# Optimization experiments

Hardware: AMD Instinct MI355X
Metric: run time of the kernel (lower is better)

Reference implementation:

```python
import jax, jax.numpy as jnp
import numpy as np
import math

N, B, S = 2048, 4, 1024
SFZ, IFZ, H, A = 384, 256, 8, 64
LN_EPS = 1e-5


def setup_inputs() -> dict:
    key = jax.random.key(0)
    ks = jax.random.split(key, 12)
    x = jax.random.normal(ks[0], (N, IFZ), dtype=jnp.float32)
    emb = jax.random.normal(ks[1], (B, S, SFZ), dtype=jnp.float32)
    mask = jax.random.randint(ks[2], (B, S), 0, 2).astype(bool)
    batch = jnp.sort(jax.random.randint(ks[3], (N,), 0, B)).astype(jnp.int64)
    sc = 1.0 / math.sqrt(IFZ)
    scs = 1.0 / math.sqrt(SFZ)
    Wq = jax.random.normal(ks[4], (IFZ, H * A), dtype=jnp.float32) * sc
    Wk = jax.random.normal(ks[5], (SFZ, H * A), dtype=jnp.float32) * scs
    Wv = jax.random.normal(ks[6], (SFZ, H * A), dtype=jnp.float32) * scs
    Wg = jax.random.normal(ks[7], (IFZ, H * A), dtype=jnp.float32) * sc
    bg = jnp.zeros((H * A,), dtype=jnp.float32)
    Wback = jax.random.normal(ks[8], (H * A, IFZ), dtype=jnp.float32) / math.sqrt(H * A)
    bback = jnp.zeros((IFZ,), dtype=jnp.float32)
    gamma = jnp.ones((IFZ,), dtype=jnp.float32)
    beta = jnp.zeros((IFZ,), dtype=jnp.float32)
    return {"x": x, "packed_sequence_emb": emb, "packed_sequence_mask": mask,
            "batch": batch, "Wq": Wq, "Wk": Wk, "Wv": Wv, "Wg": Wg, "bg": bg,
            "Wback": Wback, "bback": bback, "gamma": gamma, "beta": beta}


def _masked_softmax(scores, mask):
    # scores: [N,S,H], mask: [N,S,1] bool; softmax over S with padded entries zeroed
    neg = jnp.finfo(scores.dtype).min
    s = jnp.where(mask, scores, neg)
    s = s - jnp.max(s, axis=1, keepdims=True)
    e = jnp.exp(s) * mask
    return e / (jnp.sum(e, axis=1, keepdims=True) + 1e-9)


def reference(x, packed_sequence_emb, packed_sequence_mask, batch,
              Wq, Wk, Wv, Wg, bg, Wback, bback, gamma, beta):
    scale = math.sqrt(A)
    q = (x @ Wq).reshape(N, H, A)                               # [N,H,A]
    k = (packed_sequence_emb @ Wk).reshape(B, S, H, A)          # [B,S,H,A]
    v = (packed_sequence_emb @ Wv).reshape(B, S, H, A)
    # scores per (node, candidate-batch), then gather node's own batch entry;
    # avoids materializing k[batch] of shape [N,S,H,A]
    scores_all = jnp.einsum('nha,bsha->nbsh', q, k) / scale     # [N,B,S,H]
    idx = batch[:, None, None, None].astype(jnp.int32)
    scores = jnp.take_along_axis(scores_all, idx, axis=1)[:, 0]  # [N,S,H]
    bmask = packed_sequence_mask[batch][..., None]               # [N,S,1]
    w = _masked_softmax(scores, bmask)                           # [N,S,H]
    feat_all = jnp.einsum('nsh,bsha->nbha', w, v)                # [N,B,H,A]
    feat = jnp.take_along_axis(feat_all, idx, axis=1)[:, 0]      # [N,H,A]
    gate = jax.nn.sigmoid(x @ Wg + bg).reshape(N, H, A)
    new = (gate * feat).reshape(N, H * A) @ Wback + bback        # [N,IFZ]
    y = math.sqrt(2.0) * x + new
    mu = jnp.mean(y, axis=-1, keepdims=True)
    var = jnp.mean((y - mu) ** 2, axis=-1, keepdims=True)
    out = (y - mu) * jax.lax.rsqrt(var + LN_EPS) * gamma + beta
    seq_aa_logits = jnp.sum(scores[..., :2], axis=-1)            # [N,S]
    return out, seq_aa_logits
```

## Files before the change

### kernel.cpp

```cpp
#include <hip/hip_runtime.h>
#include <hip/hip_bf16.h>

#define NND 2048
#define BBATCH 4
#define SS 1024
#define SFZ 384
#define IFZ 256
#define HH 8
#define AA 64
#define HA 512
#define NBX 48
#define NSPL 8

typedef __attribute__((ext_vector_type(8))) short bf16x8;
typedef __attribute__((ext_vector_type(4))) float f32x4;

__device__ __forceinline__ unsigned short f2bf(float f) {
    union { float f; unsigned u; } a; a.f = f;
    unsigned r = a.u + 0x7fffu + ((a.u >> 16) & 1u);
    return (unsigned short)(r >> 16);
}
__device__ __forceinline__ float bf2f(unsigned short u) {
    return __uint_as_float((unsigned)u << 16);
}

__device__ __forceinline__ bf16x8 cvt8(const float* __restrict__ p) {
    const float4 f0 = *(const float4*)p;
    const float4 f1 = *(const float4*)(p + 4);
    bf16x8 o;
    o[0] = (short)f2bf(f0.x); o[1] = (short)f2bf(f0.y);
    o[2] = (short)f2bf(f0.z); o[3] = (short)f2bf(f0.w);
    o[4] = (short)f2bf(f1.x); o[5] = (short)f2bf(f1.y);
    o[6] = (short)f2bf(f1.z); o[7] = (short)f2bf(f1.w);
    return o;
}

__device__ __forceinline__ void tile_transpose(
    const float* __restrict__ src, unsigned short* __restrict__ dst,
    int K, int N, int kt, int nt, int t)
{
    __shared__ unsigned short tile[64][65];
    const int k0 = kt * 64, n0 = nt * 64;
    const int tr = t >> 6, tc = t & 63;
    #pragma unroll
    for (int r = 0; r < 16; ++r)
        tile[tr + r*4][tc] = f2bf(src[(size_t)(k0 + tr + r*4) * N + n0 + tc]);
    __syncthreads();
    #pragma unroll
    for (int r = 0; r < 16; ++r)
        dst[(size_t)(n0 + tr + r*4) * K + k0 + tc] = tile[tc][tr + r*4];
}

__global__ __launch_bounds__(256) void prep_kernel(
    const float* __restrict__ Wk, const float* __restrict__ Wv,
    const float* __restrict__ Wq, const float* __restrict__ Wg,
    const float* __restrict__ Wback,
    const void* __restrict__ mask_raw, const void* __restrict__ batch_raw,
    unsigned short* __restrict__ WkT, unsigned short* __restrict__ WvT,
    unsigned short* __restrict__ WqT, unsigned short* __restrict__ WgT,
    unsigned short* __restrict__ WbackT,
    float* __restrict__ mask_f, int* __restrict__ seg)
{
    const int bx = blockIdx.x, t = threadIdx.x;
    if (bx < 48)  { tile_transpose(Wk, WkT, SFZ, HA, bx/8, bx%8, t); return; }
    if (bx < 96)  { const int i = bx-48;  tile_transpose(Wv, WvT, SFZ, HA, i/8, i%8, t); return; }
    if (bx < 128) { const int i = bx-96;  tile_transpose(Wq, WqT, IFZ, HA, i/8, i%8, t); return; }
    if (bx < 160) { const int i = bx-128; tile_transpose(Wg, WgT, IFZ, HA, i/8, i%8, t); return; }
    if (bx < 192) { const int i = bx-160; tile_transpose(Wback, WbackT, HA, IFZ, i/4, i%4, t); return; }
    __shared__ int fl[4];
    __shared__ int fb;
    __shared__ int cnt[4];
    if (t < 4) { fl[t] = 0; cnt[t] = 0; }
    if (t == 0) fb = 0;
    __syncthreads();
    const unsigned char*  mb = (const unsigned char*)mask_raw;
    const unsigned short* mh = (const unsigned short*)mask_raw;
    const unsigned int*   mw = (const unsigned int*)mask_raw;
    int f0 = 0, f1 = 0, f2 = 0, f3 = 0;
    for (int i = t; i < 2048; i += 256) {
        unsigned short h = mh[i];
        if (h == 0x3f80u) f0 = 1;
        if ((i & 1) == 0 && h != 0) f1 = 1;
    }
    for (int i = t; i < 4096; i += 256)
        if ((i & 3) != 0 && mb[i] != 0) f2 = 1;
    for (int i = t; i < 1024; i += 256)
        if ((i & 1) != 0 && mw[i] != 0) f3 = 1;
    const int* bw = (const int*)batch_raw;
    int f4 = 0;
    for (int i = t + 1; i < 2048; i += 256)
        if (bw[i] < bw[i-1]) f4 = 1;
    if (f0) atomicOr(&fl[0], 1);
    if (f1) atomicOr(&fl[1], 1);
    if (f2) atomicOr(&fl[2], 1);
    if (f3) atomicOr(&fl[3], 1);
    if (f4) atomicOr(&fb, 1);
    __syncthreads();
    int mode;
    if (fl[0])      mode = fl[1] ? 1 : 0;
    else if (fl[2]) mode = 2;
    else if (fl[3]) mode = 3;
    else            mode = 4;
    for (int s = t; s < BBATCH*SS; s += 256) {
        int m;
        switch (mode) {
            case 0:  m = (mw[s]   != 0); break;
            case 1:  m = (mh[s]   != 0); break;
            case 2:  m = (mb[s]   != 0); break;
            case 3:  m = (mw[s]   != 0); break;
            default: m = (mw[2*s] != 0); break;
        }
        mask_f[s] = m ? 1.0f : 0.0f;
    }
    const int b64 = fb;
    for (int i = t; i < NND; i += 256) {
        const int bv = (b64 ? bw[2*i] : bw[i]) & 3;
        atomicAdd(&cnt[bv], 1);
    }
    __syncthreads();
    if (t == 0) {
        int s = 0;
        for (int b = 0; b < 4; ++b) { seg[2*b] = s; s += cnt[b]; seg[2*b+1] = s; }
    }
}

__global__ __launch_bounds__(256) void proj_mfma(
    const float* __restrict__ emb, const float* __restrict__ x,
    const unsigned short* __restrict__ WkT, const unsigned short* __restrict__ WvT,
    const unsigned short* __restrict__ WqT, const unsigned short* __restrict__ WgT,
    const float* __restrict__ bg,
    unsigned short* __restrict__ k_blk, unsigned short* __restrict__ v_bf,
    unsigned short* __restrict__ q_bf, float* __restrict__ gate_ws)
{
    const int t = threadIdx.x, w = t >> 6, lane = t & 63;
    const int m16 = lane & 15, quad = lane >> 4;
    const int bx = blockIdx.x;
    if (bx < 512) {
        const int r0 = (bx >> 1) * 16;
        const int b = r0 >> 10, srow = r0 & (SS - 1);
        const float* ap = emb + (size_t)(r0 + m16) * SFZ + quad * 8;
        bf16x8 af[12];
        #pragma unroll
        for (int j = 0; j < 12; ++j) af[j] = cvt8(ap + j * 32);
        if ((bx & 1) == 0) {
            #pragma unroll
            for (int nt = 0; nt < 8; ++nt) {
                const int n0 = w * 128 + nt * 16;
                const unsigned short* bp = WkT + (size_t)(n0 + m16) * SFZ + quad * 8;
                f32x4 d = (f32x4){0.f, 0.f, 0.f, 0.f};
                #pragma unroll
                for (int j = 0; j < 12; ++j)
                    d = __builtin_amdgcn_mfma_f32_16x16x32_bf16(af[j], *(const bf16x8*)(bp + j * 32), d, 0, 0, 0);
                const int head = n0 >> 6, coff = (n0 & 63) + m16;
                unsigned short* kb = k_blk + (((size_t)(b * HH + head)) * SS) * 64 + coff;
                #pragma unroll
                for (int r = 0; r < 4; ++r)
                    kb[(size_t)(srow + quad * 4 + r) * 64] = f2bf(d[r]);
            }
        } else {
            #pragma unroll
            for (int nt = 0; nt < 8; ++nt) {
                const int n0 = w * 128 + nt * 16;
                const unsigned short* bp = WvT + (size_t)(n0 + m16) * SFZ + quad * 8;
                f32x4 d = (f32x4){0.f, 0.f, 0.f, 0.f};
                #pragma unroll
                for (int j = 0; j < 12; ++j)
                    d = __builtin_amdgcn_mfma_f32_16x16x32_bf16(af[j], *(const bf16x8*)(bp + j * 32), d, 0, 0, 0);
                #pragma unroll
                for (int r = 0; r < 4; ++r)
                    v_bf[(size_t)(r0 + quad * 4 + r) * HA + n0 + m16] = f2bf(d[r]);
            }
        }
    } else {
        const int i = bx - 512;
        const int r0 = (i >> 2) * 16;
        const int tensor = (i & 3) >> 1, half = i & 1;
        const unsigned short* Wt = tensor ? WgT : WqT;
        const float* ap = x + (size_t)(r0 + m16) * IFZ + quad * 8;
        bf16x8 af[8];
        #pragma unroll
        for (int j = 0; j < 8; ++j) af[j] = cvt8(ap + j * 32);
        #pragma unroll
        for (int nt = 0; nt < 4; ++nt) {
            const int n0 = half * 256 + w * 64 + nt * 16;
            const unsigned short* bp = Wt + (size_t)(n0 + m16) * IFZ + quad * 8;
            f32x4 d = (f32x4){0.f, 0.f, 0.f, 0.f};
            #pragma unroll
            for (int j = 0; j < 8; ++j)
                d = __builtin_amdgcn_mfma_f32_16x16x32_bf16(af[j], *(const bf16x8*)(bp + j * 32), d, 0, 0, 0);
            if (tensor == 0) {
                #pragma unroll
                for (int r = 0; r < 4; ++r)
                    q_bf[(size_t)(r0 + quad * 4 + r) * HA + n0 + m16] = f2bf(d[r]);
            } else {
                const float bgv = bg[n0 + m16];
                #pragma unroll
                for (int r = 0; r < 4; ++r)
                    gate_ws[(size_t)(r0 + quad * 4 + r) * HA + n0 + m16] =
                        1.f / (1.f + __expf(-(d[r] + bgv)));
            }
        }
    }
}

__global__ __launch_bounds__(256) void transpose_v(
    const unsigned short* __restrict__ v_bf, unsigned short* __restrict__ vT_bf)
{
    __shared__ unsigned short tile[64][65];
    const int t = threadIdx.x;
    const int s0 = blockIdx.x * 64, c0 = blockIdx.y * 64, b = blockIdx.z;
    const int tr = t >> 6, tc = t & 63;
    #pragma unroll
    for (int r = 0; r < 16; ++r)
        tile[tr + r*4][tc] = v_bf[(size_t)(b * SS + s0 + tr + r*4) * HA + c0 + tc];
    __syncthreads();
    #pragma unroll
    for (int r = 0; r < 16; ++r)
        vT_bf[((size_t)b * HA + c0 + tr + r*4) * SS + s0 + tc] = tile[tc][tr + r*4];
}

__global__ __launch_bounds__(256) void attn_kernel(
    const unsigned short* __restrict__ k_blk, const unsigned short* __restrict__ vT_bf,
    const unsigned short* __restrict__ q_bf, const float* __restrict__ mask_f,
    const int* __restrict__ seg, unsigned short* __restrict__ part_O,
    float2* __restrict__ part_ml, float* __restrict__ out_logits)
{
    __shared__ unsigned short P_lds[4][16][136];
    __shared__ float raw[2][16][132];
    const int bid = blockIdx.x;
    const int xcd = bid & 7;
    const int b   = xcd >> 1;
    const int idx = (bid >> 3) * 2 + (xcd & 1);
    const int z    = idx & 15;
    const int xblk = idx >> 4;
    const int hz    = z >> 3;
    const int split = z & 7;
    const int n0 = seg[2*b] + xblk * 16;
    const int nend = seg[2*b + 1];
    if (n0 >= nend) return;
    const int nvalid = min(16, nend - n0);

    const int t = threadIdx.x;
    const int w = t >> 6, lane = t & 63;
    const int m16 = lane & 15, quad = lane >> 4;
    const int h = hz * 4 + w;
    const int s0 = split * 128;

    int nq = n0 + m16; if (nq >= nend) nq = nend - 1;
    const unsigned short* qp = q_bf + (size_t)nq * HA + h * AA + quad * 8;
    const bf16x8 qa0 = *(const bf16x8*)qp;
    const bf16x8 qa1 = *(const bf16x8*)(qp + 32);

    const unsigned short* kb = k_blk + ((size_t)(b * HH + h)) * SS * 64;
    const unsigned short* vb = vT_bf + ((size_t)b * HA + h * AA) * SS;
    unsigned short (*Pw)[136] = P_lds[w];

    float msk[8];
    #pragma unroll
    for (int st = 0; st < 8; ++st)
        msk[st] = mask_f[b * SS + s0 + st * 16 + m16];

    f32x4 d[8];
    #pragma unroll
    for (int st = 0; st < 8; ++st) {
        const unsigned short* kp = kb + (size_t)(s0 + st * 16 + m16) * 64 + quad * 8;
        const bf16x8 b0 = *(const bf16x8*)kp;
        const bf16x8 b1 = *(const bf16x8*)(kp + 32);
        f32x4 acc = (f32x4){0.f, 0.f, 0.f, 0.f};
        acc = __builtin_amdgcn_mfma_f32_16x16x32_bf16(qa0, b0, acc, 0, 0, 0);
        acc = __builtin_amdgcn_mfma_f32_16x16x32_bf16(qa1, b1, acc, 0, 0, 0);
        #pragma unroll
        for (int r = 0; r < 4; ++r) acc[r] *= 0.125f;
        d[st] = acc;
    }
    if (hz == 0) {
        if (w < 2) {
            #pragma unroll
            for (int st = 0; st < 8; ++st)
                #pragma unroll
                for (int r = 0; r < 4; ++r)
                    raw[w][quad * 4 + r][st * 16 + m16] = d[st][r];
        }
        __syncthreads();
        for (int i = t; i < 16 * 128; i += 256) {
            const int node = i >> 7, sp = i & 127;
            if (node < nvalid)
                out_logits[(size_t)(n0 + node) * SS + s0 + sp] =
                    raw[0][node][sp] + raw[1][node][sp];
        }
    }
    float m_s[4], l_s[4];
    #pragma unroll
    for (int r = 0; r < 4; ++r) {
        float mx = -3.0e38f;
        #pragma unroll
        for (int st = 0; st < 8; ++st)
            mx = (msk[st] > 0.5f) ? fmaxf(mx, d[st][r]) : mx;
        mx = fmaxf(mx, __shfl_xor(mx, 1));
        mx = fmaxf(mx, __shfl_xor(mx, 2));
        mx = fmaxf(mx, __shfl_xor(mx, 4));
        mx = fmaxf(mx, __shfl_xor(mx, 8));
        m_s[r] = mx;
        float cs = 0.f;
        #pragma unroll
        for (int st = 0; st < 8; ++st) {
            const float e = (msk[st] > 0.5f) ? __expf(d[st][r] - mx) : 0.f;
            d[st][r] = e;
            cs += e;
        }
        cs += __shfl_xor(cs, 1);
        cs += __shfl_xor(cs, 2);
        cs += __shfl_xor(cs, 4);
        cs += __shfl_xor(cs, 8);
        l_s[r] = cs;
    }
    #pragma unroll
    for (int st = 0; st < 8; ++st)
        #pragma unroll
        for (int r = 0; r < 4; ++r)
            Pw[quad * 4 + r][st * 16 + m16] = f2bf(d[st][r]);
    f32x4 facc[4];
    #pragma unroll
    for (int a = 0; a < 4; ++a) facc[a] = (f32x4){0.f, 0.f, 0.f, 0.f};
    #pragma unroll
    for (int sub = 0; sub < 4; ++sub) {
        const bf16x8 pa = *(const bf16x8*)&Pw[m16][sub * 32 + quad * 8];
        const unsigned short* vp0 = vb + (size_t)m16 * SS + s0 + sub * 32 + quad * 8;
        #pragma unroll
        for (int a = 0; a < 4; ++a) {
            const bf16x8 vfr = *(const bf16x8*)(vp0 + (size_t)(a * 16) * SS);
            facc[a] = __builtin_amdgcn_mfma_f32_16x16x32_bf16(pa, vfr, facc[a], 0, 0, 0);
        }
    }
    unsigned short* po = part_O + (size_t)split * NND * HA;
    #pragma unroll
    for (int a = 0; a < 4; ++a)
        #pragma unroll
        for (int r = 0; r < 4; ++r) {
            const int row = quad * 4 + r;
            if (row < nvalid)
                po[(size_t)(n0 + row) * HA + h * AA + a * 16 + m16] = f2bf(facc[a][r]);
        }
    if (m16 == 0) {
        #pragma unroll
        for (int r = 0; r < 4; ++r) {
            const int row = quad * 4 + r;
            if (row < nvalid)
                part_ml[(size_t)split * NND * HH + (size_t)(n0 + row) * HH + h] =
                    make_float2(m_s[r], l_s[r]);
        }
    }
}

__global__ __launch_bounds__(256) void back_ln_fused(
    const unsigned short* __restrict__ part_O, const float2* __restrict__ part_ml,
    const float* __restrict__ gate_ws, const unsigned short* __restrict__ WbackT,
    const float* __restrict__ x, const float* __restrict__ bback,
    const float* __restrict__ gamma, const float* __restrict__ beta,
    float* __restrict__ out)
{
    __shared__ float coef[NSPL][8][8];
    __shared__ unsigned short gf_l[8][520];
    __shared__ float nl[8][260];
    const int t = threadIdx.x, w = t >> 6, lane = t & 63;
    const int m16 = lane & 15, quad = lane >> 4;
    const int r0 = blockIdx.x * 8;
    if (t < 64) {
        const int row = t >> 3, h = t & 7, n = r0 + row;
        float2 ml[NSPL];
        #pragma unroll
        for (int s = 0; s < NSPL; ++s)
            ml[s] = part_ml[(size_t)s * NND * HH + (size_t)n * HH + h];
        float M = -3.0e38f;
        #pragma unroll
        for (int s = 0; s < NSPL; ++s) M = fmaxf(M, ml[s].x);
        float L = 0.f;
        float e[NSPL];
        #pragma unroll
        for (int s = 0; s < NSPL; ++s) { e[s] = __expf(ml[s].x - M); L += ml[s].y * e[s]; }
        const float invL = 1.f / (L + 1e-9f);
        #pragma unroll
        for (int s = 0; s < NSPL; ++s) coef[s][row][h] = e[s] * invL;
    }
    __syncthreads();
    #pragma unroll
    for (int it = 0; it < 4; ++it) {
        const int i = (t + it * 256) * 4;
        const int row = i >> 9, c = i & (HA - 1), h = c >> 6;
        const int n = r0 + row;
        float4 o = make_float4(0.f, 0.f, 0.f, 0.f);
        #pragma unroll
        for (int s = 0; s < NSPL; ++s) {
            const ushort4 p = *(const ushort4*)&part_O[(size_t)s * NND * HA + (size_t)n * HA + c];
            const float cf = coef[s][row][h];
            o.x = fmaf(bf2f(p.x), cf, o.x); o.y = fmaf(bf2f(p.y), cf, o.y);
            o.z = fmaf(bf2f(p.z), cf, o.z); o.w = fmaf(bf2f(p.w), cf, o.w);
        }
        const float4 g = *(const float4*)&gate_ws[(size_t)n * HA + c];
        ushort4 ob;
        ob.x = f2bf(g.x * o.x); ob.y = f2bf(g.y * o.y);
        ob.z = f2bf(g.z * o.z); ob.w = f2bf(g.w * o.w);
        *(ushort4*)&gf_l[row][c] = ob;
    }
    __syncthreads();
    bf16x8 af[16];
    #pragma unroll
    for (int j = 0; j < 16; ++j)
        af[j] = *(const bf16x8*)&gf_l[m16 & 7][quad * 8 + j * 32];
    #pragma unroll
    for (int nt = 0; nt < 4; ++nt) {
        const int n0 = w * 64 + nt * 16;
        const unsigned short* bp = WbackT + (size_t)(n0 + m16) * HA + quad * 8;
        f32x4 d = (f32x4){0.f, 0.f, 0.f, 0.f};
        #pragma unroll
        for (int j = 0; j < 16; ++j)
            d = __builtin_amdgcn_mfma_f32_16x16x32_bf16(af[j], *(const bf16x8*)(bp + j * 32), d, 0, 0, 0);
        const float bb = bback[n0 + m16];
        #pragma unroll
        for (int r = 0; r < 4; ++r) {
            const int rr = quad * 4 + r;
            if (rr < 8) nl[rr][n0 + m16] = d[r] + bb;
        }
    }
    __syncthreads();
    const int row = t >> 5, li = t & 31;
    const float* xr = x + (size_t)(r0 + row) * IFZ;
    float yv[8];
    float s1 = 0.f, s2 = 0.f;
    #pragma unroll
    for (int j = 0; j < 8; ++j) {
        const int c = li + j * 32;
        const float v = fmaf(1.41421356237309515f, xr[c], nl[row][c]);
        yv[j] = v; s1 += v; s2 += v * v;
    }
    #pragma unroll
    for (int off = 16; off >= 1; off >>= 1) {
        s1 += __shfl_xor(s1, off);
        s2 += __shfl_xor(s2, off);
    }
    const float mu  = s1 * (1.f / IFZ);
    const float var = s2 * (1.f / IFZ) - mu * mu;
    const float rv  = rsqrtf(var + 1e-5f);
    float* orow = out + (size_t)(r0 + row) * IFZ;
    #pragma unroll
    for (int j = 0; j < 8; ++j) {
        const int c = li + j * 32;
        orow[c] = (yv[j] - mu) * rv * gamma[c] + beta[c];
    }
}

extern "C" void kernel_launch(void* const* d_in, const int* in_sizes, int n_in,
                              void* d_out, int out_size, void* d_ws, size_t ws_size,
                              hipStream_t stream) {
    const float* x     = (const float*)d_in[0];
    const float* emb   = (const float*)d_in[1];
    const void*  mraw  = d_in[2];
    const void*  braw  = d_in[3];
    const float* Wq    = (const float*)d_in[4];
    const float* Wk    = (const float*)d_in[5];
    const float* Wv    = (const float*)d_in[6];
    const float* Wg    = (const float*)d_in[7];
    const float* bg    = (const float*)d_in[8];
    const float* Wback = (const float*)d_in[9];
    const float* bback = (const float*)d_in[10];
    const float* gamma = (const float*)d_in[11];
    const float* beta  = (const float*)d_in[12];

    char* ws = (char*)d_ws;
    const size_t MB = 1048576;
    size_t off = 0;
    float*          mask_f  = (float*)(ws + off);  off += 16384;
    int*            seg     = (int*)(ws + off);    off += 16384;
    unsigned short* WkT     = (unsigned short*)(ws + off); off += 393216;
    unsigned short* WvT     = (unsigned short*)(ws + off); off += 393216;
    unsigned short* WqT     = (unsigned short*)(ws + off); off += 262144;
    unsigned short* WgT     = (unsigned short*)(ws + off); off += 262144;
    unsigned short* WbackT  = (unsigned short*)(ws + off); off += 262144;
    unsigned short* k_blk   = (unsigned short*)(ws + off); off += 4*MB;
    unsigned short* v_bf    = (unsigned short*)(ws + off); off += 4*MB;
    unsigned short* vT_bf   = (unsigned short*)(ws + off); off += 4*MB;
    unsigned short* q_bf    = (unsigned short*)(ws + off); off += 2*MB;
    float*          gate_ws = (float*)(ws + off); off += 4*MB;
    unsigned short* part_O  = (unsigned short*)(ws + off); off += 16*MB;
    float2*         part_ml = (float2*)(ws + off); off += 1*MB;

    float* out        = (float*)d_out;
    float* out_logits = out + (size_t)NND * IFZ;

    hipLaunchKernelGGL(prep_kernel, dim3(193), dim3(256), 0, stream,
                       Wk, Wv, Wq, Wg, Wback, mraw, braw,
                       WkT, WvT, WqT, WgT, WbackT, mask_f, seg);
    hipLaunchKernelGGL(proj_mfma, dim3(1024), dim3(256), 0, stream,
                       emb, x, WkT, WvT, WqT, WgT, bg, k_blk, v_bf, q_bf, gate_ws);
    hipLaunchKernelGGL(transpose_v, dim3(16, 8, 4), dim3(256), 0, stream, v_bf, vT_bf);
    hipLaunchKernelGGL(attn_kernel, dim3(BBATCH * NBX * 16), dim3(256), 0, stream,
                       k_blk, vT_bf, q_bf, mask_f, seg, part_O, part_ml, out_logits);
    hipLaunchKernelGGL(back_ln_fused, dim3(NND / 8), dim3(256), 0, stream,
                       part_O, part_ml, gate_ws, WbackT, x, bback, gamma, beta, out);
}
```

Baseline: 201.5 us.

## Fuse V transpose into projection kernel and compute logits head-1 scores in-warp

The V projection now writes its 16-row tile into shared memory and stores it transposed straight to vT_bf, removing the separate transpose_v launch and the intermediate v_bf buffer. In the attention kernel, the sequence logits no longer go through an LDS staging buffer and block barrier. Warp 0 of the head-group-0 blocks recomputes head 1's scores itself and writes the head-0 plus head-1 sum directly. This trades a kernel launch, a global round trip and an LDS sync for extra MFMA work and K loads in one warp, plus narrow 16-element column stores.

New measurement: 204.3 us. About the same (+1.4%).

```diff
diff --git a/kernel.cpp b/kernel.cpp
--- a/kernel.cpp
+++ b/kernel.cpp
@@ -129,9 +129,10 @@
     const unsigned short* __restrict__ WkT, const unsigned short* __restrict__ WvT,
     const unsigned short* __restrict__ WqT, const unsigned short* __restrict__ WgT,
     const float* __restrict__ bg,
-    unsigned short* __restrict__ k_blk, unsigned short* __restrict__ v_bf,
+    unsigned short* __restrict__ k_blk, unsigned short* __restrict__ vT_bf,
     unsigned short* __restrict__ q_bf, float* __restrict__ gate_ws)
 {
+    __shared__ unsigned short v_l[16][520];
     const int t = threadIdx.x, w = t >> 6, lane = t & 63;
     const int m16 = lane & 15, quad = lane >> 4;
     const int bx = blockIdx.x;
@@ -168,7 +169,16 @@
                     d = __builtin_amdgcn_mfma_f32_16x16x32_bf16(af[j], *(const bf16x8*)(bp + j * 32), d, 0, 0, 0);
                 #pragma unroll
                 for (int r = 0; r < 4; ++r)
-                    v_bf[(size_t)(r0 + quad * 4 + r) * HA + n0 + m16] = f2bf(d[r]);
+                    v_l[quad * 4 + r][n0 + m16] = f2bf(d[r]);
+            }
+            __syncthreads();
+            for (int c = t; c < HA; c += 256) {
+                unsigned short tmp[16];
+                #pragma unroll
+                for (int s = 0; s < 16; ++s) tmp[s] = v_l[s][c];
+                unsigned short* dst = vT_bf + ((size_t)b * HA + c) * SS + srow;
+                *(uint4*)dst       = ((const uint4*)tmp)[0];
+                *(uint4*)(dst + 8) = ((const uint4*)tmp)[1];
             }
         }
     } else {
@@ -203,22 +213,6 @@
     }
 }
 
-__global__ __launch_bounds__(256) void transpose_v(
-    const unsigned short* __restrict__ v_bf, unsigned short* __restrict__ vT_bf)
-{
-    __shared__ unsigned short tile[64][65];
-    const int t = threadIdx.x;
-    const int s0 = blockIdx.x * 64, c0 = blockIdx.y * 64, b = blockIdx.z;
-    const int tr = t >> 6, tc = t & 63;
-    #pragma unroll
-    for (int r = 0; r < 16; ++r)
-        tile[tr + r*4][tc] = v_bf[(size_t)(b * SS + s0 + tr + r*4) * HA + c0 + tc];
-    __syncthreads();
-    #pragma unroll
-    for (int r = 0; r < 16; ++r)
-        vT_bf[((size_t)b * HA + c0 + tr + r*4) * SS + s0 + tc] = tile[tc][tr + r*4];
-}
-
 __global__ __launch_bounds__(256) void attn_kernel(
     const unsigned short* __restrict__ k_blk, const unsigned short* __restrict__ vT_bf,
     const unsigned short* __restrict__ q_bf, const float* __restrict__ mask_f,
@@ -226,7 +220,6 @@
     float2* __restrict__ part_ml, float* __restrict__ out_logits)
 {
     __shared__ unsigned short P_lds[4][16][136];
-    __shared__ float raw[2][16][132];
     const int bid = blockIdx.x;
     const int xcd = bid & 7;
     const int b   = xcd >> 1;
@@ -273,20 +266,24 @@
         for (int r = 0; r < 4; ++r) acc[r] *= 0.125f;
         d[st] = acc;
     }
-    if (hz == 0) {
-        if (w < 2) {
+    if (hz == 0 && w == 0) {
+        const unsigned short* qp1 = q_bf + (size_t)nq * HA + AA + quad * 8;
+        const bf16x8 qb0 = *(const bf16x8*)qp1;
+        const bf16x8 qb1 = *(const bf16x8*)(qp1 + 32);
+        const unsigned short* kb1 = k_blk + ((size_t)(b * HH + 1)) * SS * 64;
+        #pragma unroll
+        for (int st = 0; st < 8; ++st) {
+            const unsigned short* kp = kb1 + (size_t)(s0 + st * 16 + m16) * 64 + quad * 8;
+            f32x4 acc = (f32x4){0.f, 0.f, 0.f, 0.f};
+            acc = __builtin_amdgcn_mfma_f32_16x16x32_bf16(qb0, *(const bf16x8*)kp, acc, 0, 0, 0);
+            acc = __builtin_amdgcn_mfma_f32_16x16x32_bf16(qb1, *(const bf16x8*)(kp + 32), acc, 0, 0, 0);
             #pragma unroll
-            for (int st = 0; st < 8; ++st)
-                #pragma unroll
-                for (int r = 0; r < 4; ++r)
-                    raw[w][quad * 4 + r][st * 16 + m16] = d[st][r];
-        }
-        __syncthreads();
-        for (int i = t; i < 16 * 128; i += 256) {
-            const int node = i >> 7, sp = i & 127;
-            if (node < nvalid)
-                out_logits[(size_t)(n0 + node) * SS + s0 + sp] =
-                    raw[0][node][sp] + raw[1][node][sp];
+            for (int r = 0; r < 4; ++r) {
+                const int node = quad * 4 + r;
+                if (node < nvalid)
+                    out_logits[(size_t)(n0 + node) * SS + s0 + st * 16 + m16] =
+                        d[st][r] + acc[r] * 0.125f;
+            }
         }
     }
     float m_s[4], l_s[4];
@@ -477,7 +474,6 @@
     unsigned short* WgT     = (unsigned short*)(ws + off); off += 262144;
     unsigned short* WbackT  = (unsigned short*)(ws + off); off += 262144;
     unsigned short* k_blk   = (unsigned short*)(ws + off); off += 4*MB;
-    unsigned short* v_bf    = (unsigned short*)(ws + off); off += 4*MB;
     unsigned short* vT_bf   = (unsigned short*)(ws + off); off += 4*MB;
     unsigned short* q_bf    = (unsigned short*)(ws + off); off += 2*MB;
     float*          gate_ws = (float*)(ws + off); off += 4*MB;
@@ -491,8 +487,7 @@
                        Wk, Wv, Wq, Wg, Wback, mraw, braw,
                        WkT, WvT, WqT, WgT, WbackT, mask_f, seg);
     hipLaunchKernelGGL(proj_mfma, dim3(1024), dim3(256), 0, stream,
-                       emb, x, WkT, WvT, WqT, WgT, bg, k_blk, v_bf, q_bf, gate_ws);
-    hipLaunchKernelGGL(transpose_v, dim3(16, 8, 4), dim3(256), 0, stream, v_bf, vT_bf);
+                       emb, x, WkT, WvT, WqT, WgT, bg, k_blk, vT_bf, q_bf, gate_ws);
     hipLaunchKernelGGL(attn_kernel, dim3(BBATCH * NBX * 16), dim3(256), 0, stream,
                        k_blk, vT_bf, q_bf, mask_f, seg, part_O, part_ml, out_logits);
     hipLaunchKernelGGL(back_ln_fused, dim3(NND / 8), dim3(256), 0, stream,
```
